# Kernel optimization log

Measured on AMD Instinct MI355X. Metric: run time of the kernel, lower is better.

The kernel has to match this reference:

```python
import jax, jax.numpy as jnp
import numpy as np

B, T, D_E, D_RHO = 4, 2048, 8, 8
D_MODEL, NHEAD, NLAYERS, DFF = 128, 4, 3, 256
WINDOW = 64
LN_EPS = 1e-5


def _layernorm(x, g, b):
    mu = jnp.mean(x, axis=-1, keepdims=True)
    var = jnp.mean((x - mu) ** 2, axis=-1, keepdims=True)
    return (x - mu) * jax.lax.rsqrt(var + LN_EPS) * g + b


def _pos_encoding(t, d, dtype):
    half = d // 2
    pos = jnp.arange(t, dtype=dtype)[:, None]
    div = jnp.exp(jnp.arange(half, dtype=dtype) * (-jnp.log(jnp.asarray(10000.0, dtype)) / half))
    ang = pos * div[None, :]  # (T, half)
    pe = jnp.zeros((t, d), dtype=dtype)
    pe = pe.at[:, 0:2 * half:2].set(jnp.sin(ang))
    pe = pe.at[:, 1:2 * half:2].set(jnp.cos(ang))
    return pe[None]  # (1, T, d)


def setup_inputs() -> dict:
    key = jax.random.key(0)
    ks = iter(jax.random.split(key, 32))
    d_in = D_E + D_RHO

    def lin(k, fan_in, shape):
        return jax.random.uniform(k, shape, jnp.float32, -1.0, 1.0) / np.sqrt(fan_in)

    inp = {
        'E': jax.random.normal(next(ks), (B, T, D_E), jnp.float32),
        'rho_side': jax.random.normal(next(ks), (B, T, D_RHO), jnp.float32),
        'W_in1': lin(next(ks), d_in, (d_in, D_MODEL)), 'b_in1': jnp.zeros((D_MODEL,)),
        'W_in2': lin(next(ks), D_MODEL, (D_MODEL, D_MODEL)), 'b_in2': jnp.zeros((D_MODEL,)),
        'Wqkv': lin(next(ks), D_MODEL, (NLAYERS, D_MODEL, 3 * D_MODEL)), 'bqkv': jnp.zeros((NLAYERS, 3 * D_MODEL)),
        'Wo': lin(next(ks), D_MODEL, (NLAYERS, D_MODEL, D_MODEL)), 'bo': jnp.zeros((NLAYERS, D_MODEL)),
        'ln1_g': jnp.ones((NLAYERS, D_MODEL)), 'ln1_b': jnp.zeros((NLAYERS, D_MODEL)),
        'Wff1': lin(next(ks), D_MODEL, (NLAYERS, D_MODEL, DFF)), 'bff1': jnp.zeros((NLAYERS, DFF)),
        'Wff2': lin(next(ks), DFF, (NLAYERS, DFF, D_MODEL)), 'bff2': jnp.zeros((NLAYERS, D_MODEL)),
        'ln2_g': jnp.ones((NLAYERS, D_MODEL)), 'ln2_b': jnp.zeros((NLAYERS, D_MODEL)),
        'W_head': lin(next(ks), D_MODEL, (D_MODEL, D_RHO)), 'b_head': jnp.zeros((D_RHO,)),
    }
    return inp


def reference(E, rho_side, W_in1, b_in1, W_in2, b_in2, Wqkv, bqkv, Wo, bo,
              ln1_g, ln1_b, Wff1, bff1, Wff2, bff2, ln2_g, ln2_b, W_head, b_head):
    b, t, _ = E.shape
    x = jnp.concatenate([E, rho_side], axis=-1)  # (B,T,d_e+d_rho)
    # in_proj: Linear -> ReLU -> Linear, then add sinusoidal PE (layernorm_in=False)
    h = jax.nn.relu(x @ W_in1 + b_in1) @ W_in2 + b_in2
    h = h + _pos_encoding(t, D_MODEL, h.dtype)

    # banded causal mask: blocked if j > i or j < i - window + 1 (additive -inf)
    i = jnp.arange(t)[:, None]
    j = jnp.arange(t)[None, :]
    blocked = (j > i) | (j < i - WINDOW + 1)
    bias = jnp.where(blocked, -jnp.inf, 0.0).astype(h.dtype)[None, None]  # (1,1,T,T)

    hd = D_MODEL // NHEAD
    scale = 1.0 / np.sqrt(hd)
    for l in range(NLAYERS):
        # --- self-attention (post-norm TransformerEncoderLayer, dropout=0) ---
        qkv = h @ Wqkv[l] + bqkv[l]
        q, k, v = jnp.split(qkv, 3, axis=-1)
        q = q.reshape(b, t, NHEAD, hd)
        k = k.reshape(b, t, NHEAD, hd)
        v = v.reshape(b, t, NHEAD, hd)
        scores = jnp.einsum('bqhd,bkhd->bhqk', q, k) * scale + bias
        attn = jax.nn.softmax(scores, axis=-1)
        o = jnp.einsum('bhqk,bkhd->bqhd', attn, v).reshape(b, t, D_MODEL)
        h = _layernorm(h + o @ Wo[l] + bo[l], ln1_g[l], ln1_b[l])
        # --- feed-forward ---
        ff = jax.nn.relu(h @ Wff1[l] + bff1[l]) @ Wff2[l] + bff2[l]
        h = _layernorm(h + ff, ln2_g[l], ln2_b[l])

    return h @ W_head + b_head  # (B,T,d_rho)
```

## Files before the change

### kernel.cpp

```cpp
#include <hip/hip_runtime.h>
#include <hip/hip_bf16.h>
#include <math.h>

#define TSEQ 2048
#define NBATCH 4
#define NTOK (TSEQ * NBATCH)
#define DM 128
#define WIN 64
#define DFF 256
#define NQKV 384
#define QT 64

typedef __attribute__((ext_vector_type(8))) short bf16x8;
typedef __attribute__((ext_vector_type(4))) float f32x4;

__device__ __forceinline__ unsigned short f2bf(float f) {
    union { float f; unsigned int u; } v; v.f = f;
    unsigned int r = v.u + 0x7fffu + ((v.u >> 16) & 1u);
    return (unsigned short)(r >> 16);
}
__device__ __forceinline__ float bf2f_lo(unsigned int u) {
    union { unsigned int u; float f; } v; v.u = u << 16; return v.f;
}
__device__ __forceinline__ float bf2f_hi(unsigned int u) {
    union { unsigned int u; float f; } v; v.u = u & 0xffff0000u; return v.f;
}

__global__ void k_wconv(const float* __restrict__ Wqkv, const float* __restrict__ Wo,
                        const float* __restrict__ Wff1, const float* __restrict__ Wff2,
                        unsigned short* __restrict__ wq, unsigned short* __restrict__ wo,
                        unsigned short* __restrict__ w1, unsigned short* __restrict__ w2) {
    int idx = blockIdx.x * 256 + threadIdx.x;
    const int s1 = 3 * 128 * 384, s2 = 3 * 128 * 128, s3 = 3 * 128 * 256, s4 = 3 * 256 * 128;
    if (idx < s1) {
        int l = idx / (384 * 128), rem = idx % (384 * 128);
        int n = rem / 128, k = rem % 128;
        wq[idx] = f2bf(Wqkv[(size_t)l * 128 * 384 + k * 384 + n]);
    } else if ((idx -= s1) < s2) {
        int l = idx / (128 * 128), rem = idx % (128 * 128);
        int n = rem / 128, k = rem % 128;
        wo[idx] = f2bf(Wo[(size_t)l * 128 * 128 + k * 128 + n]);
    } else if ((idx -= s2) < s3) {
        int l = idx / (256 * 128), rem = idx % (256 * 128);
        int n = rem / 128, k = rem % 128;
        w1[idx] = f2bf(Wff1[(size_t)l * 128 * 256 + k * 256 + n]);
    } else if ((idx -= s3) < s4) {
        int l = idx / (128 * 256), rem = idx % (128 * 256);
        int n = rem / 256, k = rem % 256;
        w2[idx] = f2bf(Wff2[(size_t)l * 256 * 128 + k * 128 + n]);
    }
}

template<int ROWS>
__global__ void k_inproj(const float* __restrict__ E, const float* __restrict__ rho,
                         const float* __restrict__ W1, const float* __restrict__ b1,
                         const float* __restrict__ W2, const float* __restrict__ b2,
                         float* __restrict__ h, unsigned short* __restrict__ hbf) {
    const int row0 = blockIdx.x * ROWS;
    const int tid = threadIdx.x;
    __shared__ float x[ROWS][16];
    __shared__ float h1[ROWS][DM];

    for (int idx = tid; idx < ROWS * 16; idx += DM) {
        int r = idx >> 4, c = idx & 15;
        int tok = row0 + r;
        x[r][c] = (c < 8) ? E[(size_t)tok * 8 + c] : rho[(size_t)tok * 8 + (c - 8)];
    }
    __syncthreads();

    float acc[ROWS];
#pragma unroll
    for (int r = 0; r < ROWS; ++r) acc[r] = b1[tid];
    for (int k = 0; k < 16; ++k) {
        float w = W1[k * DM + tid];
#pragma unroll
        for (int r = 0; r < ROWS; ++r) acc[r] += x[r][k] * w;
    }
#pragma unroll
    for (int r = 0; r < ROWS; ++r) h1[r][tid] = fmaxf(acc[r], 0.f);
    __syncthreads();

#pragma unroll
    for (int r = 0; r < ROWS; ++r) acc[r] = b2[tid];
    for (int k = 0; k < DM; ++k) {
        float w = W2[k * DM + tid];
#pragma unroll
        for (int r = 0; r < ROWS; ++r) acc[r] += h1[r][k] * w;
    }

    const float c0 = -0.14391156831212787f;
    float dv = __expf(c0 * (float)(tid >> 1));
#pragma unroll
    for (int r = 0; r < ROWS; ++r) {
        int tok = row0 + r;
        int t = tok & (TSEQ - 1);
        float ang = (float)t * dv;
        float pe = (tid & 1) ? cosf(ang) : sinf(ang);
        float v = acc[r] + pe;
        h[(size_t)tok * DM + tid] = v;
        hbf[(size_t)tok * DM + tid] = f2bf(v);
    }
}

template<int K, int N, bool RELU, bool OUTBF16>
__global__ __launch_bounds__(256) void k_gemm_mfma(
        const unsigned short* __restrict__ A,
        const unsigned short* __restrict__ Wt,
        const float* __restrict__ bias,
        void* __restrict__ Cout) {
    const int bm0 = blockIdx.x * 64;
    const int bn0 = blockIdx.y * 64;
    const int w = threadIdx.x >> 6;
    const int l = threadIdx.x & 63;
    const int lr = l & 15;
    const int lk = l >> 4;
    const int arow = bm0 + w * 16 + lr;

    bf16x8 aF[K / 32];
    const unsigned short* ap = A + (size_t)arow * K + lk * 8;
#pragma unroll
    for (int ks = 0; ks < K / 32; ++ks)
        aF[ks] = *(const bf16x8*)(ap + ks * 32);

    f32x4 acc[4];
#pragma unroll
    for (int nt = 0; nt < 4; ++nt) {
        float b = bias[bn0 + nt * 16 + lr];
        acc[nt][0] = b; acc[nt][1] = b; acc[nt][2] = b; acc[nt][3] = b;
    }

#pragma unroll
    for (int ks = 0; ks < K / 32; ++ks) {
#pragma unroll
        for (int nt = 0; nt < 4; ++nt) {
            const unsigned short* bp = Wt + (size_t)(bn0 + nt * 16 + lr) * K + ks * 32 + lk * 8;
            bf16x8 bF = *(const bf16x8*)bp;
            acc[nt] = __builtin_amdgcn_mfma_f32_16x16x32_bf16(aF[ks], bF, acc[nt], 0, 0, 0);
        }
    }

#pragma unroll
    for (int nt = 0; nt < 4; ++nt) {
        int col = bn0 + nt * 16 + lr;
#pragma unroll
        for (int r = 0; r < 4; ++r) {
            int row = bm0 + w * 16 + lk * 4 + r;
            float v = acc[nt][r];
            if (RELU) v = fmaxf(v, 0.f);
            if (OUTBF16) ((unsigned short*)Cout)[(size_t)row * N + col] = f2bf(v);
            else ((float*)Cout)[(size_t)row * N + col] = v;
        }
    }
}

template<int K>
__global__ __launch_bounds__(128) void k_gemm_ln(
        const unsigned short* __restrict__ A,
        const unsigned short* __restrict__ Wt,
        const float* __restrict__ bias,
        const float* __restrict__ g, const float* __restrict__ be,
        float* __restrict__ h, unsigned short* __restrict__ hbf) {
    const int bm0 = blockIdx.x * 32;
    const int w = threadIdx.x >> 6;
    const int l = threadIdx.x & 63;
    const int lr = l & 15;
    const int lk = l >> 4;
    const int arow = bm0 + w * 16 + lr;

    bf16x8 aF[K / 32];
    const unsigned short* ap = A + (size_t)arow * K + lk * 8;
#pragma unroll
    for (int ks = 0; ks < K / 32; ++ks)
        aF[ks] = *(const bf16x8*)(ap + ks * 32);

    f32x4 acc[8];
#pragma unroll
    for (int nt = 0; nt < 8; ++nt) {
        float b = bias[nt * 16 + lr];
        acc[nt][0] = b; acc[nt][1] = b; acc[nt][2] = b; acc[nt][3] = b;
    }

#pragma unroll
    for (int ks = 0; ks < K / 32; ++ks) {
#pragma unroll
        for (int nt = 0; nt < 8; ++nt) {
            const unsigned short* bp = Wt + (size_t)(nt * 16 + lr) * K + ks * 32 + lk * 8;
            bf16x8 bF = *(const bf16x8*)bp;
            acc[nt] = __builtin_amdgcn_mfma_f32_16x16x32_bf16(aF[ks], bF, acc[nt], 0, 0, 0);
        }
    }

#pragma unroll
    for (int nt = 0; nt < 8; ++nt) {
        int col = nt * 16 + lr;
#pragma unroll
        for (int r = 0; r < 4; ++r) {
            int row = bm0 + w * 16 + lk * 4 + r;
            acc[nt][r] += h[(size_t)row * DM + col];
        }
    }

    float s[4], s2[4];
#pragma unroll
    for (int r = 0; r < 4; ++r) {
        float a0 = 0.f, a1 = 0.f;
#pragma unroll
        for (int nt = 0; nt < 8; ++nt) { a0 += acc[nt][r]; a1 += acc[nt][r] * acc[nt][r]; }
        s[r] = a0; s2[r] = a1;
    }
#pragma unroll
    for (int off = 8; off; off >>= 1) {
#pragma unroll
        for (int r = 0; r < 4; ++r) {
            s[r]  += __shfl_xor(s[r],  off);
            s2[r] += __shfl_xor(s2[r], off);
        }
    }
    float mean[4], rstd[4];
#pragma unroll
    for (int r = 0; r < 4; ++r) {
        mean[r] = s[r] * (1.f / DM);
        float var = s2[r] * (1.f / DM) - mean[r] * mean[r];
        rstd[r] = rsqrtf(var + 1e-5f);
    }

#pragma unroll
    for (int nt = 0; nt < 8; ++nt) {
        int col = nt * 16 + lr;
        float gg = g[col], bb = be[col];
#pragma unroll
        for (int r = 0; r < 4; ++r) {
            int row = bm0 + w * 16 + lk * 4 + r;
            float v = (acc[nt][r] - mean[r]) * rstd[r] * gg + bb;
            h[(size_t)row * DM + col] = v;
            hbf[(size_t)row * DM + col] = f2bf(v);
        }
    }
}

__global__ void k_attn2(const unsigned short* __restrict__ qkv, unsigned short* __restrict__ o) {
    const int t0   = blockIdx.x * QT;
    const int head = blockIdx.y;
    const int b    = blockIdx.z;
    const int tid  = threadIdx.x;
    const int q    = tid >> 2;
    const int s    = tid & 3;

    __shared__ float kbuf[127][36];
    __shared__ float vbuf[127][36];

    for (int idx = tid; idx < 127 * 4; idx += 256) {
        int kb = idx >> 2, c = idx & 3;
        int j = t0 - 63 + kb;
        uint4 kv = make_uint4(0, 0, 0, 0), vv = make_uint4(0, 0, 0, 0);
        if (j >= 0) {
            const unsigned short* base = qkv + ((size_t)(b * TSEQ + j)) * NQKV + head * 32 + c * 8;
            kv = *(const uint4*)(base + 128);
            vv = *(const uint4*)(base + 256);
        }
        float* kd = &kbuf[kb][c * 8];
        float* vd = &vbuf[kb][c * 8];
        kd[0] = bf2f_lo(kv.x); kd[1] = bf2f_hi(kv.x); kd[2] = bf2f_lo(kv.y); kd[3] = bf2f_hi(kv.y);
        kd[4] = bf2f_lo(kv.z); kd[5] = bf2f_hi(kv.z); kd[6] = bf2f_lo(kv.w); kd[7] = bf2f_hi(kv.w);
        vd[0] = bf2f_lo(vv.x); vd[1] = bf2f_hi(vv.x); vd[2] = bf2f_lo(vv.y); vd[3] = bf2f_hi(vv.y);
        vd[4] = bf2f_lo(vv.z); vd[5] = bf2f_hi(vv.z); vd[6] = bf2f_lo(vv.w); vd[7] = bf2f_hi(vv.w);
    }

    float qreg[32];
    {
        const unsigned short* qp = qkv + ((size_t)(b * TSEQ + t0 + q)) * NQKV + head * 32;
#pragma unroll
        for (int c = 0; c < 4; ++c) {
            uint4 u = *(const uint4*)(qp + c * 8);
            float* qd = &qreg[c * 8];
            qd[0] = bf2f_lo(u.x); qd[1] = bf2f_hi(u.x); qd[2] = bf2f_lo(u.y); qd[3] = bf2f_hi(u.y);
            qd[4] = bf2f_lo(u.z); qd[5] = bf2f_hi(u.z); qd[6] = bf2f_lo(u.w); qd[7] = bf2f_hi(u.w);
        }
    }
    __syncthreads();

    const float scale = 0.17677669529663687f;
    float sc[16];
#pragma unroll
    for (int kk = 0; kk < 16; ++kk) {
        int w = s + 4 * kk;
        int kb = q + w;
        float acc = 0.f;
#pragma unroll
        for (int d = 0; d < 32; ++d) acc += qreg[d] * kbuf[kb][d];
        int j = t0 + q - 63 + w;
        sc[kk] = (j >= 0) ? acc * scale : -1e30f;
    }

    float m = sc[0];
#pragma unroll
    for (int kk = 1; kk < 16; ++kk) m = fmaxf(m, sc[kk]);
    m = fmaxf(m, __shfl_xor(m, 1));
    m = fmaxf(m, __shfl_xor(m, 2));
    float sum = 0.f;
#pragma unroll
    for (int kk = 0; kk < 16; ++kk) { sc[kk] = __expf(sc[kk] - m); sum += sc[kk]; }
    sum += __shfl_xor(sum, 1);
    sum += __shfl_xor(sum, 2);
    const float inv = 1.f / sum;

    float acc[32];
#pragma unroll
    for (int d = 0; d < 32; ++d) acc[d] = 0.f;
#pragma unroll
    for (int kk = 0; kk < 16; ++kk) {
        float p = sc[kk] * inv;
        int kb = q + s + 4 * kk;
#pragma unroll
        for (int d = 0; d < 32; ++d) acc[d] += p * vbuf[kb][d];
    }
#pragma unroll
    for (int d = 0; d < 32; ++d) {
        acc[d] += __shfl_xor(acc[d], 1);
        acc[d] += __shfl_xor(acc[d], 2);
    }
    if (s == 0) {
        unsigned short* op = o + ((size_t)(b * TSEQ + t0 + q)) * DM + head * 32;
#pragma unroll
        for (int d = 0; d < 32; d += 2) {
            unsigned int u = ((unsigned int)f2bf(acc[d + 1]) << 16) | f2bf(acc[d]);
            *(unsigned int*)(op + d) = u;
        }
    }
}

__global__ void k_head(const float* __restrict__ h, const float* __restrict__ W,
                       const float* __restrict__ bias, float* __restrict__ out) {
    const int tok = blockIdx.x * blockDim.x + threadIdx.x;
    if (tok >= NTOK) return;
    float acc[8];
#pragma unroll
    for (int r = 0; r < 8; ++r) acc[r] = bias[r];
    for (int k = 0; k < DM; ++k) {
        float hv = h[(size_t)tok * DM + k];
#pragma unroll
        for (int r = 0; r < 8; ++r) acc[r] += hv * W[k * 8 + r];
    }
#pragma unroll
    for (int r = 0; r < 8; ++r) out[(size_t)tok * 8 + r] = acc[r];
}

extern "C" void kernel_launch(void* const* d_in, const int* in_sizes, int n_in,
                              void* d_out, int out_size, void* d_ws, size_t ws_size,
                              hipStream_t stream) {
    const float* E     = (const float*)d_in[0];
    const float* rho   = (const float*)d_in[1];
    const float* W_in1 = (const float*)d_in[2];
    const float* b_in1 = (const float*)d_in[3];
    const float* W_in2 = (const float*)d_in[4];
    const float* b_in2 = (const float*)d_in[5];
    const float* Wqkv  = (const float*)d_in[6];
    const float* bqkv  = (const float*)d_in[7];
    const float* Wo    = (const float*)d_in[8];
    const float* bo    = (const float*)d_in[9];
    const float* ln1g  = (const float*)d_in[10];
    const float* ln1b  = (const float*)d_in[11];
    const float* Wff1  = (const float*)d_in[12];
    const float* bff1  = (const float*)d_in[13];
    const float* Wff2  = (const float*)d_in[14];
    const float* bff2  = (const float*)d_in[15];
    const float* ln2g  = (const float*)d_in[16];
    const float* ln2b  = (const float*)d_in[17];
    const float* Whead = (const float*)d_in[18];
    const float* bhead = (const float*)d_in[19];
    float* out = (float*)d_out;

    char* ws = (char*)d_ws;
    const size_t MB = 1024 * 1024;
    float*          h    = (float*)ws;
    unsigned short* hbf  = (unsigned short*)(ws + 4 * MB);
    unsigned short* obf  = (unsigned short*)(ws + 6 * MB);
    unsigned short* wq   = (unsigned short*)(ws + 8 * MB);
    unsigned short* wo   = (unsigned short*)(ws + 8 * MB + 294912);
    unsigned short* w1   = (unsigned short*)(ws + 8 * MB + 294912 + 98304);
    unsigned short* w2   = (unsigned short*)(ws + 8 * MB + 294912 + 98304 + 196608);
    unsigned short* qkvb = (unsigned short*)(ws + 9 * MB);
    unsigned short* fbuf = (unsigned short*)(ws + 13 * MB);

    constexpr int ROWS = 8;
    k_wconv<<<1536, 256, 0, stream>>>(Wqkv, Wo, Wff1, Wff2, wq, wo, w1, w2);
    k_inproj<ROWS><<<NTOK / ROWS, DM, 0, stream>>>(E, rho, W_in1, b_in1, W_in2, b_in2, h, hbf);
    for (int l = 0; l < 3; ++l) {
        k_gemm_mfma<DM, NQKV, false, true><<<dim3(NTOK / 64, NQKV / 64), 256, 0, stream>>>(
            hbf, wq + (size_t)l * NQKV * DM, bqkv + l * NQKV, qkvb);
        k_attn2<<<dim3(TSEQ / QT, 4, NBATCH), 256, 0, stream>>>(qkvb, obf);
        k_gemm_ln<DM><<<NTOK / 32, 128, 0, stream>>>(
            obf, wo + (size_t)l * DM * DM, bo + l * DM, ln1g + l * DM, ln1b + l * DM, h, hbf);
        k_gemm_mfma<DM, DFF, true, true><<<dim3(NTOK / 64, DFF / 64), 256, 0, stream>>>(
            hbf, w1 + (size_t)l * DFF * DM, bff1 + l * DFF, fbuf);
        k_gemm_ln<DFF><<<NTOK / 32, 128, 0, stream>>>(
            fbuf, w2 + (size_t)l * DM * DFF, bff2 + l * DM, ln2g + l * DM, ln2b + l * DM, h, hbf);
    }
    k_head<<<NTOK / 256, 256, 0, stream>>>(h, Whead, bhead, out);
}
```

Measured before the change: 295.8 us.

## Fuse FFN up-projection, ReLU, down-projection and LayerNorm into one kernel

Replaces the separate FF1 GEMM kernel and the FF2+LayerNorm kernel with a single kernel per 32-row tile. The ReLU'd intermediate activations are stored as bf16 in shared memory and never go to global memory. This removes one launch per layer and the global write and read of the 8192x256 intermediate buffer. In exchange each block holds 16 accumulator tiles in registers and reads weights straight from global/L2, which may lower occupancy.

```diff
diff --git a/kernel.cpp b/kernel.cpp
--- a/kernel.cpp
+++ b/kernel.cpp
@@ -232,6 +232,128 @@
         for (int r = 0; r < 4; ++r) {
             int row = bm0 + w * 16 + lk * 4 + r;
             float v = (acc[nt][r] - mean[r]) * rstd[r] * gg + bb;
+            h[(size_t)row * DM + col] = v;
+            hbf[(size_t)row * DM + col] = f2bf(v);
+        }
+    }
+}
+
+__global__ __launch_bounds__(128) void k_ff_fused(
+        const unsigned short* __restrict__ A,
+        const unsigned short* __restrict__ W1t,
+        const float* __restrict__ b1,
+        const unsigned short* __restrict__ W2t,
+        const float* __restrict__ b2,
+        const float* __restrict__ g, const float* __restrict__ be,
+        float* __restrict__ h, unsigned short* __restrict__ hbf) {
+    const int bm0 = blockIdx.x * 32;
+    const int w = threadIdx.x >> 6;
+    const int l = threadIdx.x & 63;
+    const int lr = l & 15;
+    const int lk = l >> 4;
+
+    __shared__ unsigned short a2[32][264];
+
+    const int arow = bm0 + w * 16 + lr;
+    bf16x8 aF[4];
+    const unsigned short* ap = A + (size_t)arow * DM + lk * 8;
+#pragma unroll
+    for (int ks = 0; ks < 4; ++ks)
+        aF[ks] = *(const bf16x8*)(ap + ks * 32);
+
+    f32x4 acc[16];
+#pragma unroll
+    for (int nt = 0; nt < 16; ++nt) { acc[nt][0] = 0.f; acc[nt][1] = 0.f; acc[nt][2] = 0.f; acc[nt][3] = 0.f; }
+
+#pragma unroll
+    for (int ks = 0; ks < 4; ++ks) {
+#pragma unroll
+        for (int nt = 0; nt < 16; ++nt) {
+            const unsigned short* wp = W1t + (size_t)(nt * 16 + lr) * DM + ks * 32 + lk * 8;
+            bf16x8 wF = *(const bf16x8*)wp;
+            acc[nt] = __builtin_amdgcn_mfma_f32_16x16x32_bf16(wF, aF[ks], acc[nt], 0, 0, 0);
+        }
+    }
+
+    const int mloc = w * 16 + lr;
+#pragma unroll
+    for (int nt = 0; nt < 16; ++nt) {
+        int n0 = nt * 16 + lk * 4;
+        uint2 pk;
+        float v0 = fmaxf(acc[nt][0] + b1[n0 + 0], 0.f);
+        float v1 = fmaxf(acc[nt][1] + b1[n0 + 1], 0.f);
+        float v2 = fmaxf(acc[nt][2] + b1[n0 + 2], 0.f);
+        float v3 = fmaxf(acc[nt][3] + b1[n0 + 3], 0.f);
+        pk.x = (unsigned int)f2bf(v0) | ((unsigned int)f2bf(v1) << 16);
+        pk.y = (unsigned int)f2bf(v2) | ((unsigned int)f2bf(v3) << 16);
+        *(uint2*)&a2[mloc][n0] = pk;
+    }
+    __syncthreads();
+
+    bf16x8 aF2[8];
+#pragma unroll
+    for (int ks = 0; ks < 8; ++ks)
+        aF2[ks] = *(const bf16x8*)&a2[w * 16 + lr][ks * 32 + lk * 8];
+
+    f32x4 acc2[8];
+#pragma unroll
+    for (int nt = 0; nt < 8; ++nt) {
+        float b = b2[nt * 16 + lr];
+        acc2[nt][0] = b; acc2[nt][1] = b; acc2[nt][2] = b; acc2[nt][3] = b;
+    }
+
+#pragma unroll
+    for (int ks = 0; ks < 8; ++ks) {
+#pragma unroll
+        for (int nt = 0; nt < 8; ++nt) {
+            const unsigned short* bp = W2t + (size_t)(nt * 16 + lr) * DFF + ks * 32 + lk * 8;
+            bf16x8 bF = *(const bf16x8*)bp;
+            acc2[nt] = __builtin_amdgcn_mfma_f32_16x16x32_bf16(aF2[ks], bF, acc2[nt], 0, 0, 0);
+        }
+    }
+
+#pragma unroll
+    for (int nt = 0; nt < 8; ++nt) {
+        int col = nt * 16 + lr;
+#pragma unroll
+        for (int r = 0; r < 4; ++r) {
+            int row = bm0 + w * 16 + lk * 4 + r;
+            acc2[nt][r] += h[(size_t)row * DM + col];
+        }
+    }
+
+    float s[4], s2[4];
+#pragma unroll
+    for (int r = 0; r < 4; ++r) {
+        float a0 = 0.f, a1 = 0.f;
+#pragma unroll
+        for (int nt = 0; nt < 8; ++nt) { a0 += acc2[nt][r]; a1 += acc2[nt][r] * acc2[nt][r]; }
+        s[r] = a0; s2[r] = a1;
+    }
+#pragma unroll
+    for (int off = 8; off; off >>= 1) {
+#pragma unroll
+        for (int r = 0; r < 4; ++r) {
+            s[r]  += __shfl_xor(s[r],  off);
+            s2[r] += __shfl_xor(s2[r], off);
+        }
+    }
+    float mean[4], rstd[4];
+#pragma unroll
+    for (int r = 0; r < 4; ++r) {
+        mean[r] = s[r] * (1.f / DM);
+        float var = s2[r] * (1.f / DM) - mean[r] * mean[r];
+        rstd[r] = rsqrtf(var + 1e-5f);
+    }
+
+#pragma unroll
+    for (int nt = 0; nt < 8; ++nt) {
+        int col = nt * 16 + lr;
+        float gg = g[col], bb = be[col];
+#pragma unroll
+        for (int r = 0; r < 4; ++r) {
+            int row = bm0 + w * 16 + lk * 4 + r;
+            float v = (acc2[nt][r] - mean[r]) * rstd[r] * gg + bb;
             h[(size_t)row * DM + col] = v;
             hbf[(size_t)row * DM + col] = f2bf(v);
         }
@@ -380,7 +502,6 @@
     unsigned short* w1   = (unsigned short*)(ws + 8 * MB + 294912 + 98304);
     unsigned short* w2   = (unsigned short*)(ws + 8 * MB + 294912 + 98304 + 196608);
     unsigned short* qkvb = (unsigned short*)(ws + 9 * MB);
-    unsigned short* fbuf = (unsigned short*)(ws + 13 * MB);
 
     constexpr int ROWS = 8;
     k_wconv<<<1536, 256, 0, stream>>>(Wqkv, Wo, Wff1, Wff2, wq, wo, w1, w2);
@@ -391,10 +512,10 @@
         k_attn2<<<dim3(TSEQ / QT, 4, NBATCH), 256, 0, stream>>>(qkvb, obf);
         k_gemm_ln<DM><<<NTOK / 32, 128, 0, stream>>>(
             obf, wo + (size_t)l * DM * DM, bo + l * DM, ln1g + l * DM, ln1b + l * DM, h, hbf);
-        k_gemm_mfma<DM, DFF, true, true><<<dim3(NTOK / 64, DFF / 64), 256, 0, stream>>>(
-            hbf, w1 + (size_t)l * DFF * DM, bff1 + l * DFF, fbuf);
-        k_gemm_ln<DFF><<<NTOK / 32, 128, 0, stream>>>(
-            fbuf, w2 + (size_t)l * DM * DFF, bff2 + l * DM, ln2g + l * DM, ln2b + l * DM, h, hbf);
+        k_ff_fused<<<NTOK / 32, 128, 0, stream>>>(
+            hbf, w1 + (size_t)l * DFF * DM, bff1 + l * DFF,
+            w2 + (size_t)l * DM * DFF, bff2 + l * DM,
+            ln2g + l * DM, ln2b + l * DM, h, hbf);
     }
     k_head<<<NTOK / 256, 256, 0, stream>>>(h, Whead, bhead, out);
 }
```

New measurement: 288.7 us. -2.4%, faster.
